# Performance work log

Hardware: AMD Instinct MI355X
Metric: run time of the kernel (lower is better)

Reference implementation:

```python
import jax, jax.numpy as jnp
import numpy as np

R = 10  # num_relations
NUM_GRAPHS = 64


def rgcn_layer(x, W, root, b, src, dst, etype):
    # x: [N, Din], W: [R, Din, H], root: [Din, H], b: [H]
    N = x.shape[0]
    H = W.shape[-1]
    # per-relation transform of all nodes: [R, N, H]
    h_all = jnp.einsum('nd,rdh->rnh', x, W)
    # gather transformed source features per edge by its relation: [E, H]
    msg = h_all[etype, src]
    # mean-aggregate per (dst, relation) pair, then sum over relations (PyG RGCNConv semantics)
    key = dst * R + etype
    sums = jax.ops.segment_sum(msg, key, num_segments=N * R)  # [N*R, H]
    cnt = jax.ops.segment_sum(jnp.ones((etype.shape[0],), x.dtype), key, num_segments=N * R)
    agg = (sums.reshape(N, R, H) / jnp.clip(cnt.reshape(N, R, 1), 1.0, None)).sum(axis=1)
    return agg + x @ root + b


def setup_inputs() -> dict:
    key = jax.random.key(0)
    ks = jax.random.split(key, 12)
    N, E, DIN, H = 100000, 3200000, 128, 64
    x = jax.random.normal(ks[0], (N, DIN), dtype=jnp.float32)
    edge_index = jax.random.randint(ks[1], (2, E), 0, N, dtype=jnp.int64)
    edge_type = jax.random.randint(ks[2], (E,), 0, R, dtype=jnp.int64)
    batch = jnp.sort(jax.random.randint(ks[3], (N,), 0, NUM_GRAPHS, dtype=jnp.int64))
    s1 = 1.0 / np.sqrt(DIN)
    s2 = 1.0 / np.sqrt(H)
    W1 = jax.random.uniform(ks[4], (R, DIN, H), jnp.float32, -s1, s1)
    root1 = jax.random.uniform(ks[5], (DIN, H), jnp.float32, -s1, s1)
    b1 = jnp.zeros((H,), jnp.float32)
    W2 = jax.random.uniform(ks[6], (R, H, H), jnp.float32, -s2, s2)
    root2 = jax.random.uniform(ks[7], (H, H), jnp.float32, -s2, s2)
    b2 = jnp.zeros((H,), jnp.float32)
    cls_w = jax.random.uniform(ks[8], (H, 1), jnp.float32, -s2, s2)
    cls_b = jnp.zeros((1,), jnp.float32)
    return {"x": x, "edge_index": edge_index, "edge_type": edge_type, "batch": batch,
            "W1": W1, "root1": root1, "b1": b1, "W2": W2, "root2": root2, "b2": b2,
            "cls_w": cls_w, "cls_b": cls_b}


def reference(x, edge_index, edge_type, batch, W1, root1, b1, W2, root2, b2, cls_w, cls_b):
    src, dst = edge_index[0], edge_index[1]
    h = jax.nn.relu(rgcn_layer(x, W1, root1, b1, src, dst, edge_type))   # dropout = identity (eval)
    h = jax.nn.relu(rgcn_layer(h, W2, root2, b2, src, dst, edge_type))
    # global mean pool per graph
    sums = jax.ops.segment_sum(h, batch, num_segments=NUM_GRAPHS)        # [G, H]
    cnt = jax.ops.segment_sum(jnp.ones((h.shape[0],), h.dtype), batch, num_segments=NUM_GRAPHS)
    pooled = sums / jnp.clip(cnt[:, None], 1.0, None)
    out = pooled @ cls_w + cls_b                                          # [G, 1]
    return out.reshape(-1)
```

## Files before the change

kernel.cpp:

```cpp
#include <hip/hip_runtime.h>

#define R_REL 10
#define HD 64
#define BSH 8
#define KPB (256 * R_REL)
#define SORT_CAP 12288

typedef __attribute__((ext_vector_type(8))) short short8;
typedef __attribute__((ext_vector_type(4))) float floatx4;
typedef __attribute__((ext_vector_type(8))) unsigned short ushort8;

__device__ inline unsigned short f32_to_bf16_rne(float f) {
    unsigned int u = __float_as_uint(f);
    unsigned int r = (u + 0x7FFFu + ((u >> 16) & 1u)) >> 16;
    return (unsigned short)r;
}
__device__ inline float bf16_to_f32(unsigned short h) {
    return __uint_as_float(((unsigned int)h) << 16);
}
__device__ inline float bf16lo(unsigned int u) { return __uint_as_float(u << 16); }
__device__ inline float bf16hi(unsigned int u) { return __uint_as_float(u & 0xFFFF0000u); }

__device__ __forceinline__ void gload_lds16(const unsigned short* g, unsigned short* l) {
    __builtin_amdgcn_global_load_lds(
        (const __attribute__((address_space(1))) unsigned int*)g,
        (__attribute__((address_space(3))) unsigned int*)l, 16, 0, 0);
}

#define BAR_VMCNT(N)                                              \
    do {                                                          \
        asm volatile("s_waitcnt vmcnt(" #N ")" ::: "memory");     \
        __builtin_amdgcn_sched_barrier(0);                        \
        __builtin_amdgcn_s_barrier();                             \
        __builtin_amdgcn_sched_barrier(0);                        \
    } while (0)

__global__ __launch_bounds__(256) void bhist_kernel(const int* __restrict__ dst,
                                                    int* __restrict__ bcnt, int E) {
    __shared__ int l[512];
    int t = threadIdx.x;
    l[t] = 0; l[t + 256] = 0;
    __syncthreads();
    int e0 = blockIdx.x * 4096;
    for (int i = t; i < 4096; i += 256) {
        int e = e0 + i;
        if (e < E) atomicAdd(&l[dst[e] >> BSH], 1);
    }
    __syncthreads();
    if (l[t]) atomicAdd(&bcnt[t], l[t]);
    if (l[t + 256]) atomicAdd(&bcnt[t + 256], l[t + 256]);
}

__global__ void bscan_kernel(const int* __restrict__ bcnt, int* __restrict__ boff,
                             int* __restrict__ gcursor, int NBK, int E) {
    int t = threadIdx.x;
    int v = (t < NBK) ? bcnt[t] : 0;
    __shared__ int tmp[512];
    tmp[t] = v;
    __syncthreads();
    for (int off = 1; off < 512; off <<= 1) {
        int u = (t >= off) ? tmp[t - off] : 0;
        __syncthreads();
        tmp[t] += u;
        __syncthreads();
    }
    int excl = tmp[t] - v;
    if (t < NBK) { boff[t] = excl; gcursor[t] = excl; }
    if (t == 0) boff[NBK] = E;
}

__global__ __launch_bounds__(256) void bscatter_kernel(const int* __restrict__ src,
                                                       const int* __restrict__ dst,
                                                       const int* __restrict__ et,
                                                       int* __restrict__ gcursor,
                                                       unsigned int* __restrict__ staged,
                                                       int E) {
    __shared__ int lcnt[512];
    __shared__ int lstart[512];
    __shared__ int lbase[512];
    __shared__ int tmp[256];
    __shared__ unsigned int lbuf[4096];
    __shared__ unsigned short lbkt[4096];
    int t = threadIdx.x;
    int e0 = blockIdx.x * 4096;
    int nthis = min(4096, E - e0);
    lcnt[t] = 0; lcnt[t + 256] = 0;
    __syncthreads();
    for (int i = t; i < nthis; i += 256) atomicAdd(&lcnt[dst[e0 + i] >> BSH], 1);
    __syncthreads();
    int c0 = lcnt[2 * t], c1 = lcnt[2 * t + 1];
    int ps = c0 + c1;
    tmp[t] = ps;
    __syncthreads();
    for (int off = 1; off < 256; off <<= 1) {
        int u = (t >= off) ? tmp[t - off] : 0;
        __syncthreads();
        tmp[t] += u;
        __syncthreads();
    }
    int ex = tmp[t] - ps;
    lstart[2 * t] = ex; lstart[2 * t + 1] = ex + c0;
    lbase[2 * t]     = (c0 > 0) ? atomicAdd(&gcursor[2 * t], c0) : 0;
    lbase[2 * t + 1] = (c1 > 0) ? atomicAdd(&gcursor[2 * t + 1], c1) : 0;
    __syncthreads();
    lcnt[t] = 0; lcnt[t + 256] = 0;
    __syncthreads();
    for (int i = t; i < nthis; i += 256) {
        int dd = dst[e0 + i];
        int bk = dd >> BSH;
        int lk = (dd & ((1 << BSH) - 1)) * R_REL + et[e0 + i];
        unsigned int p = ((unsigned int)lk << 17) | (unsigned int)src[e0 + i];
        int pos = lstart[bk] + atomicAdd(&lcnt[bk], 1);
        lbuf[pos] = p; lbkt[pos] = (unsigned short)bk;
    }
    __syncthreads();
    for (int i = t; i < nthis; i += 256) {
        int bk = lbkt[i];
        staged[lbase[bk] + i - lstart[bk]] = lbuf[i];
    }
}

__global__ __launch_bounds__(256) void sortfill_kernel(const unsigned int* __restrict__ staged,
                                                       const int* __restrict__ boff,
                                                       int* __restrict__ dcnt,
                                                       int2* __restrict__ edata,
                                                       int N, int Ntot) {
    __shared__ int hist[KPB];
    __shared__ float wkey[KPB];
    __shared__ int part[256];
    __shared__ int lsrc[SORT_CAP];
    __shared__ unsigned short lkey[SORT_CAP];
    int t = threadIdx.x, b = blockIdx.x;
    int s0 = boff[b], s1 = boff[b + 1];
#pragma unroll
    for (int j = 0; j < KPB / 256; ++j) hist[t + j * 256] = 0;
    __syncthreads();
    for (int i = s0 + t; i < s1; i += 256)
        atomicAdd(&hist[staged[i] >> 17], 1);
    __syncthreads();
    int base = t * (KPB / 256);
    int c[KPB / 256];
    int s = 0;
#pragma unroll
    for (int j = 0; j < KPB / 256; ++j) {
        c[j] = hist[base + j]; s += c[j];
        wkey[base + j] = 1.0f / fmaxf((float)c[j], 1.0f);
    }
    int dglob = b * 256 + t;
    if (dglob < Ntot) dcnt[dglob] = s;
    part[t] = s;
    __syncthreads();
    for (int off = 1; off < 256; off <<= 1) {
        int u = (t >= off) ? part[t - off] : 0;
        __syncthreads();
        part[t] += u;
        __syncthreads();
    }
    int run = part[t] - s;
#pragma unroll
    for (int j = 0; j < KPB / 256; ++j) { hist[base + j] = run; run += c[j]; }
    __syncthreads();
    for (int i = s0 + t; i < s1; i += 256) {
        unsigned int p = staged[i];
        int lk = p >> 17;
        int pos = atomicAdd(&hist[lk], 1);
        if (pos < SORT_CAP) { lsrc[pos] = (int)(p & 0x1FFFFu); lkey[pos] = (unsigned short)lk; }
        else {
            int rel = lk % R_REL;
            edata[s0 + pos] = make_int2(rel * N + (int)(p & 0x1FFFFu), __float_as_int(wkey[lk]));
        }
    }
    __syncthreads();
    int m = min(s1 - s0, SORT_CAP);
    for (int j = t; j < m; j += 256) {
        int lk = lkey[j];
        int rel = lk % R_REL;
        edata[s0 + j] = make_int2(rel * N + lsrc[j], __float_as_int(wkey[lk]));
    }
}

__global__ void scan1_kernel(const int* __restrict__ cnt, int* __restrict__ bsum, int M) {
    int b = blockIdx.x, tid = threadIdx.x;
    int base = b * 1024 + tid * 4;
    int s = 0;
#pragma unroll
    for (int j = 0; j < 4; ++j) { int i = base + j; if (i < M) s += cnt[i]; }
    for (int off = 32; off > 0; off >>= 1) s += __shfl_down(s, off);
    __shared__ int wsum[4];
    int lane = tid & 63, wid = tid >> 6;
    if (lane == 0) wsum[wid] = s;
    __syncthreads();
    if (tid == 0) bsum[b] = wsum[0] + wsum[1] + wsum[2] + wsum[3];
}

__global__ void scan2_kernel(const int* __restrict__ bsum, int* __restrict__ boff, int NB) {
    int tid = threadIdx.x;
    int lane = tid & 63, wid = tid >> 6;
    int v = (tid < NB) ? bsum[tid] : 0;
    int x = v;
    for (int off = 1; off < 64; off <<= 1) { int u = __shfl_up(x, off); if (lane >= off) x += u; }
    __shared__ int wsum[16];
    if (lane == 63) wsum[wid] = x;
    __syncthreads();
    int woff = 0;
    for (int w = 0; w < wid; ++w) woff += wsum[w];
    if (tid < NB) boff[tid] = x + woff - v;
}

__global__ void scan3_kernel(const int* __restrict__ cnt, const int* __restrict__ boff,
                             int* __restrict__ rowptr, int M) {
    int b = blockIdx.x, tid = threadIdx.x;
    int base = b * 1024 + tid * 4;
    int c[4]; int s = 0;
#pragma unroll
    for (int j = 0; j < 4; ++j) { int i = base + j; c[j] = (i < M) ? cnt[i] : 0; s += c[j]; }
    int lane = tid & 63, wid = tid >> 6;
    int x = s;
    for (int off = 1; off < 64; off <<= 1) { int u = __shfl_up(x, off); if (lane >= off) x += u; }
    __shared__ int wsum[4];
    if (lane == 63) wsum[wid] = x;
    __syncthreads();
    int woff = 0;
    for (int w = 0; w < wid; ++w) woff += wsum[w];
    int run = boff[b] + x + woff - s;
#pragma unroll
    for (int j = 0; j < 4; ++j) {
        int i = base + j;
        if (i < M) {
            rowptr[i] = run; run += c[j];
            if (i == M - 1) rowptr[M] = run;
        }
    }
}

__global__ void split_kernel(const float* __restrict__ src, unsigned short* __restrict__ hi,
                             unsigned short* __restrict__ lo, int n) {
    int i = blockIdx.x * 256 + threadIdx.x;
    if (i < n) {
        float v = src[i];
        unsigned short h = f32_to_bf16_rne(v);
        hi[i] = h;
        lo[i] = f32_to_bf16_rne(v - bf16_to_f32(h));
    }
}

__global__ void wsplit_kernel(const float* __restrict__ W, const float* __restrict__ root,
                              unsigned short* __restrict__ hi, int K) {
    int idx = blockIdx.x * 256 + threadIdx.x;
    int total = (R_REL + 1) * HD * K;
    if (idx >= total) return;
    int rel = idx / (HD * K);
    int rem = idx - rel * HD * K;
    int n = rem / K, k = rem - n * K;
    float v = (rel < R_REL) ? W[((size_t)rel * K + k) * HD + n] : root[(size_t)k * HD + n];
    int ks = k ^ ((n & 7) << 3);
    hi[rel * HD * K + n * K + ks] = f32_to_bf16_rne(v);
}

template <int K>
__global__ __launch_bounds__(512, 6)
void gemm_mfma(const unsigned short* __restrict__ Xhi,
               const unsigned short* __restrict__ Xlo,
               const unsigned short* __restrict__ Wthi,
               unsigned short* __restrict__ hout,
               float* __restrict__ fout, int N) {
    constexpr int NS = K / 32;
    constexpr int TILE_SH = HD * K;
    constexpr int SC = K / 64;
    __shared__ unsigned short wlds[2 * TILE_SH];
    const int tid = threadIdx.x;
    const int w = tid >> 6, lane = tid & 63;
    const int quad = lane >> 4, l16 = lane & 15;
    const int n0 = blockIdx.x * 128;
    const int node = n0 + w * 16 + l16;
    const bool valid = node < N;
    const bool full = (n0 + 128 <= N);

    short8 Xh[NS], Xl[NS];
#pragma unroll
    for (int s = 0; s < NS; ++s) {
        short8 z;
#pragma unroll
        for (int q = 0; q < 8; ++q) z[q] = 0;
        Xh[s] = z; Xl[s] = z;
        if (valid) {
            Xh[s] = *(const short8*)(Xhi + (size_t)node * K + s * 32 + quad * 8);
            Xl[s] = *(const short8*)(Xlo + (size_t)node * K + s * 32 + quad * 8);
        }
    }

    auto stage = [&](int rel, int b) {
        const unsigned short* hsrc = Wthi + (size_t)rel * TILE_SH;
        unsigned short* dst0 = wlds + b * TILE_SH;
#pragma unroll
        for (int j = 0; j < SC; ++j) {
            int q = j * 8 + w;
            gload_lds16(hsrc + q * 512 + lane * 8, dst0 + q * 512);
        }
    };

    stage(0, 0);
    BAR_VMCNT(0);

    const int swzb = (l16 & 7) << 4;
    const size_t NHD = (size_t)N * HD;

#pragma unroll
    for (int c = 0; c <= R_REL; ++c) {
        const int cur = c & 1;
        if (c < R_REL) stage(c + 1, cur ^ 1);
        const char* wb = (const char*)(wlds + cur * TILE_SH);
        floatx4 acc[4];
#pragma unroll
        for (int mt = 0; mt < 4; ++mt) { floatx4 z = {0.f, 0.f, 0.f, 0.f}; acc[mt] = z; }
#pragma unroll
        for (int s = 0; s < NS; ++s) {
            const int koffb = ((s * 32 + quad * 8) * 2) ^ swzb;
#pragma unroll
            for (int mt = 0; mt < 4; ++mt) {
                const int rowb = (mt * 16 + l16) * (K * 2);
                short8 Wh = *(const short8*)(wb + rowb + koffb);
                acc[mt] = __builtin_amdgcn_mfma_f32_16x16x32_bf16(Wh, Xh[s], acc[mt], 0, 0, 0);
                acc[mt] = __builtin_amdgcn_mfma_f32_16x16x32_bf16(Wh, Xl[s], acc[mt], 0, 0, 0);
            }
        }
        if (c < R_REL) {
            if (valid) {
                unsigned short* hp = hout + (size_t)c * NHD + (size_t)node * HD;
#pragma unroll
                for (int mt = 0; mt < 4; ++mt) {
                    unsigned int d0 = (unsigned int)f32_to_bf16_rne(acc[mt][0]) |
                                      ((unsigned int)f32_to_bf16_rne(acc[mt][1]) << 16);
                    unsigned int d1 = (unsigned int)f32_to_bf16_rne(acc[mt][2]) |
                                      ((unsigned int)f32_to_bf16_rne(acc[mt][3]) << 16);
                    *(uint2*)(hp + mt * 16 + quad * 4) = make_uint2(d0, d1);
                }
            }
        } else {
            if (valid) {
                float* fp = fout + (size_t)node * HD;
#pragma unroll
                for (int mt = 0; mt < 4; ++mt)
                    *(floatx4*)(fp + mt * 16 + quad * 4) = acc[mt];
            }
        }
        if (c < R_REL) {
            if (full) BAR_VMCNT(4); else BAR_VMCNT(0);
        }
    }
}

__global__ __launch_bounds__(256) void agg_kernel(const unsigned short* __restrict__ hc,
                                                  const int* __restrict__ rowptr,
                                                  const int2* __restrict__ edata,
                                                  float* __restrict__ acc, int N) {
    int gid = blockIdx.x * 256 + threadIdx.x;
    int d = gid >> 6;
    if (d >= N) return;
    int lane = threadIdx.x & 63;
    int quarter = lane >> 4, l16 = lane & 15;
    int e0 = rowptr[d], e1 = rowptr[d + 1];
    int ne = e1 - e0;
    if (ne == 0) return;
    float s0 = 0.f, s1 = 0.f, s2 = 0.f, s3 = 0.f;
    for (int rb = 0; rb < ne; rb += 64) {
        int nthis = min(64, ne - rb);
        int2 ed = make_int2(0, 0);
        if (lane < nthis) ed = edata[e0 + rb + lane];
        int off = ed.x << 6;
        float wv = __int_as_float(ed.y);
        for (int j = 0; j < nthis; j += 8) {
            int   oa = __shfl(off, j + quarter);
            float wa = __shfl(wv,  j + quarter);
            int   ob = __shfl(off, j + 4 + quarter);
            float wb = __shfl(wv,  j + 4 + quarter);
            uint2 da = *(const uint2*)(hc + oa + l16 * 4);
            uint2 db = *(const uint2*)(hc + ob + l16 * 4);
            s0 += wa * bf16lo(da.x); s1 += wa * bf16hi(da.x);
            s2 += wa * bf16lo(da.y); s3 += wa * bf16hi(da.y);
            s0 += wb * bf16lo(db.x); s1 += wb * bf16hi(db.x);
            s2 += wb * bf16lo(db.y); s3 += wb * bf16hi(db.y);
        }
    }
    s0 += __shfl_xor(s0, 16); s1 += __shfl_xor(s1, 16);
    s2 += __shfl_xor(s2, 16); s3 += __shfl_xor(s3, 16);
    s0 += __shfl_xor(s0, 32); s1 += __shfl_xor(s1, 32);
    s2 += __shfl_xor(s2, 32); s3 += __shfl_xor(s3, 32);
    if (lane < 16) {
        float4* ap = (float4*)(acc + (size_t)d * HD + l16 * 4);
        float4 a = *ap;
        a.x += s0; a.y += s1; a.z += s2; a.w += s3;
        *ap = a;
    }
}

__global__ void fin1_kernel(const float* __restrict__ acc, const float* __restrict__ bias,
                            unsigned short* __restrict__ hi, unsigned short* __restrict__ lo,
                            int NH) {
    int i = blockIdx.x * 256 + threadIdx.x;
    if (i < NH) {
        float v = fmaxf(acc[i] + bias[i & (HD - 1)], 0.f);
        unsigned short h = f32_to_bf16_rne(v);
        hi[i] = h;
        lo[i] = f32_to_bf16_rne(v - bf16_to_f32(h));
    }
}

__global__ __launch_bounds__(256) void pool_kernel(const float* __restrict__ acc,
                                                   const float* __restrict__ bias,
                                                   const int* __restrict__ batch,
                                                   float* __restrict__ pooled,
                                                   float* __restrict__ gcnt, int N) {
    int w = blockIdx.x * 4 + (threadIdx.x >> 6);
    int lane = threadIdx.x & 63;
    int base = w * 64;
    if (base >= N) return;
    int nn = min(64, N - base);
    float b = bias[lane];
    int g_l = (base + lane < N) ? batch[base + lane] : -1;
    int g_first = __shfl(g_l, 0);
    int g_last = __shfl(g_l, nn - 1);
    if (nn == 64 && g_first == g_last) {
        float p0 = 0.f, p1 = 0.f, p2 = 0.f, p3 = 0.f;
#pragma unroll
        for (int i = 0; i < 64; i += 4) {
            p0 += fmaxf(acc[(size_t)(base + i + 0) * HD + lane] + b, 0.f);
            p1 += fmaxf(acc[(size_t)(base + i + 1) * HD + lane] + b, 0.f);
            p2 += fmaxf(acc[(size_t)(base + i + 2) * HD + lane] + b, 0.f);
            p3 += fmaxf(acc[(size_t)(base + i + 3) * HD + lane] + b, 0.f);
        }
        atomicAdd(&pooled[g_first * HD + lane], (p0 + p1) + (p2 + p3));
        if (lane == 0) atomicAdd(&gcnt[g_first], 64.f);
    } else {
        int cur = g_first; float s = 0.f; int cnt = 0;
        for (int i = 0; i < nn; ++i) {
            int g = __shfl(g_l, i);
            if (g != cur) {
                atomicAdd(&pooled[cur * HD + lane], s);
                if (lane == 0) atomicAdd(&gcnt[cur], (float)cnt);
                cur = g; s = 0.f; cnt = 0;
            }
            s += fmaxf(acc[(size_t)(base + i) * HD + lane] + b, 0.f);
            cnt++;
        }
        atomicAdd(&pooled[cur * HD + lane], s);
        if (lane == 0) atomicAdd(&gcnt[cur], (float)cnt);
    }
}

__global__ void cls_kernel(const float* __restrict__ pooled, const float* __restrict__ gcnt,
                           const float* __restrict__ cls_w, const float* __restrict__ cls_b,
                           float* __restrict__ out) {
    int g = threadIdx.x;
    float invc = 1.0f / fmaxf(gcnt[g], 1.0f);
    float acc = 0.f;
    for (int j = 0; j < 64; ++j) acc += pooled[g * 64 + j] * cls_w[j];
    out[g] = acc * invc + cls_b[0];
}

extern "C" void kernel_launch(void* const* d_in, const int* in_sizes, int n_in,
                              void* d_out, int out_size, void* d_ws, size_t ws_size,
                              hipStream_t stream) {
    const float* x     = (const float*)d_in[0];
    const int*   eidx  = (const int*)d_in[1];
    const int*   et    = (const int*)d_in[2];
    const int*   batch = (const int*)d_in[3];
    const float* W1    = (const float*)d_in[4];
    const float* root1 = (const float*)d_in[5];
    const float* b1    = (const float*)d_in[6];
    const float* W2    = (const float*)d_in[7];
    const float* root2 = (const float*)d_in[8];
    const float* b2    = (const float*)d_in[9];
    const float* cls_w = (const float*)d_in[10];
    const float* cls_b = (const float*)d_in[11];

    const int N = in_sizes[3];
    const int E = in_sizes[2];
    const int NB = (N + 1023) / 1024;
    const int NBK = (N + (1 << BSH) - 1) >> BSH;
    const int* srcp = eidx;
    const int* dstp = eidx + E;

    char* ws = (char*)d_ws;
    size_t off = 0;
    auto alloc = [&](size_t bytes) -> void* {
        void* p = ws + off;
        off = (off + bytes + 255) & ~(size_t)255;
        return p;
    };
    unsigned short* Xhi  = (unsigned short*)alloc((size_t)N * 128 * 2);
    unsigned short* Xlo  = (unsigned short*)alloc((size_t)N * 128 * 2);
    float*          accb = (float*)alloc((size_t)N * HD * 4);
    unsigned short* Wt1hi = (unsigned short*)alloc((size_t)(R_REL + 1) * HD * 128 * 2);
    unsigned short* Wt2hi = (unsigned short*)alloc((size_t)(R_REL + 1) * HD * HD * 2);
    int2*  edata  = (int2*)alloc((size_t)E * 8);
    int*   rowptr = (int*)alloc((size_t)(N + 1) * 4);
    int*   dcnt   = (int*)alloc((size_t)N * 4);
    int*   bsum   = (int*)alloc((size_t)NB * 4);
    int*   bofs   = (int*)alloc((size_t)NB * 4);
    int*   bcnt   = (int*)alloc(512 * 4);
    int*   bboff  = (int*)alloc(513 * 4);
    int*   gcur   = (int*)alloc(512 * 4);
    float* pooled = (float*)alloc((size_t)(64 * HD + 64) * 4);
    float* gcnt   = pooled + 64 * HD;
    unsigned short* h_chunk = (unsigned short*)alloc((size_t)R_REL * N * HD * 2);

    unsigned int* staged = (unsigned int*)Xhi;
    unsigned short* H1hi = Xhi;
    unsigned short* H1lo = Xlo;

    hipMemsetAsync(bcnt, 0, 512 * 4, stream);
    hipMemsetAsync(pooled, 0, (size_t)(64 * HD + 64) * 4, stream);

    int nchunks = (E + 4095) / 4096;
    bhist_kernel<<<nchunks, 256, 0, stream>>>(dstp, bcnt, E);
    bscan_kernel<<<1, 512, 0, stream>>>(bcnt, bboff, gcur, NBK, E);
    bscatter_kernel<<<nchunks, 256, 0, stream>>>(srcp, dstp, et, gcur, staged, E);
    sortfill_kernel<<<NBK, 256, 0, stream>>>(staged, bboff, dcnt, edata, N, N);
    scan1_kernel<<<NB, 256, 0, stream>>>(dcnt, bsum, N);
    scan2_kernel<<<1, 1024, 0, stream>>>(bsum, bofs, NB);
    scan3_kernel<<<NB, 256, 0, stream>>>(dcnt, bofs, rowptr, N);

    int NK = N * 128;
    split_kernel<<<(NK + 255) / 256, 256, 0, stream>>>(x, Xhi, Xlo, NK);
    int tw1 = (R_REL + 1) * HD * 128, tw2 = (R_REL + 1) * HD * HD;
    wsplit_kernel<<<(tw1 + 255) / 256, 256, 0, stream>>>(W1, root1, Wt1hi, 128);
    wsplit_kernel<<<(tw2 + 255) / 256, 256, 0, stream>>>(W2, root2, Wt2hi, HD);

    const int gemmBlocks = (N + 127) / 128;
    const int aggBlocks  = (int)(((size_t)N * 64 + 255) / 256);
    const int NH = N * HD;

    gemm_mfma<128><<<gemmBlocks, 512, 0, stream>>>(Xhi, Xlo, Wt1hi, h_chunk, accb, N);
    agg_kernel<<<aggBlocks, 256, 0, stream>>>(h_chunk, rowptr, edata, accb, N);
    fin1_kernel<<<(NH + 255) / 256, 256, 0, stream>>>(accb, b1, H1hi, H1lo, NH);

    gemm_mfma<64><<<gemmBlocks, 512, 0, stream>>>(H1hi, H1lo, Wt2hi, h_chunk, accb, N);
    agg_kernel<<<aggBlocks, 256, 0, stream>>>(h_chunk, rowptr, edata, accb, N);

    int poolWaves = (N + 63) / 64;
    pool_kernel<<<(poolWaves + 3) / 4, 256, 0, stream>>>(accb, b2, batch, pooled, gcnt, N);
    cls_kernel<<<1, 64, 0, stream>>>(pooled, gcnt, cls_w, cls_b, (float*)d_out);
}
```

Baseline: 570.2 us.

## Compress edge records and fuse bias/ReLU/split and pooling into aggregation

Edge records shrink from 8-byte (offset, weight) pairs to a packed 4-byte (relation, src) word. The mean weights move into a per-(dst, relation) table that each wave loads once and shares across lanes by shuffle. The aggregation kernel now applies bias and ReLU directly. In layer 1 it writes the bf16 hi/lo split, and in layer 2 it atomically adds into the pooled sums, which removes the separate fin1 and pool kernels and a full pass over the accumulator. Graph counts come from a small new kernel. The trade-off is one atomic per node-feature into only 64 graph rows, which may contend heavily.

```diff
diff --git a/kernel.cpp b/kernel.cpp
--- a/kernel.cpp
+++ b/kernel.cpp
@@ -123,10 +123,10 @@
 __global__ __launch_bounds__(256) void sortfill_kernel(const unsigned int* __restrict__ staged,
                                                        const int* __restrict__ boff,
                                                        int* __restrict__ dcnt,
-                                                       int2* __restrict__ edata,
+                                                       unsigned int* __restrict__ edata,
+                                                       float* __restrict__ wrow,
                                                        int N, int Ntot) {
     __shared__ int hist[KPB];
-    __shared__ float wkey[KPB];
     __shared__ int part[256];
     __shared__ int lsrc[SORT_CAP];
     __shared__ unsigned short lkey[SORT_CAP];
@@ -144,7 +144,7 @@
 #pragma unroll
     for (int j = 0; j < KPB / 256; ++j) {
         c[j] = hist[base + j]; s += c[j];
-        wkey[base + j] = 1.0f / fmaxf((float)c[j], 1.0f);
+        wrow[b * KPB + base + j] = 1.0f / fmaxf((float)c[j], 1.0f);
     }
     int dglob = b * 256 + t;
     if (dglob < Ntot) dcnt[dglob] = s;
@@ -167,7 +167,7 @@
         if (pos < SORT_CAP) { lsrc[pos] = (int)(p & 0x1FFFFu); lkey[pos] = (unsigned short)lk; }
         else {
             int rel = lk % R_REL;
-            edata[s0 + pos] = make_int2(rel * N + (int)(p & 0x1FFFFu), __float_as_int(wkey[lk]));
+            edata[s0 + pos] = ((unsigned int)rel << 20) | (p & 0x1FFFFu);
         }
     }
     __syncthreads();
@@ -175,7 +175,7 @@
     for (int j = t; j < m; j += 256) {
         int lk = lkey[j];
         int rel = lk % R_REL;
-        edata[s0 + j] = make_int2(rel * N + lsrc[j], __float_as_int(wkey[lk]));
+        edata[s0 + j] = ((unsigned int)rel << 20) | (unsigned int)lsrc[j];
     }
 }
 
@@ -255,6 +255,21 @@
     float v = (rel < R_REL) ? W[((size_t)rel * K + k) * HD + n] : root[(size_t)k * HD + n];
     int ks = k ^ ((n & 7) << 3);
     hi[rel * HD * K + n * K + ks] = f32_to_bf16_rne(v);
+}
+
+__global__ __launch_bounds__(256) void gcnt_kernel(const int* __restrict__ batch,
+                                                   float* __restrict__ gcnt, int N) {
+    __shared__ int h[64];
+    int t = threadIdx.x;
+    if (t < 64) h[t] = 0;
+    __syncthreads();
+    int i0 = blockIdx.x * 4096;
+    for (int i = t; i < 4096; i += 256) {
+        int n = i0 + i;
+        if (n < N) atomicAdd(&h[batch[n]], 1);
+    }
+    __syncthreads();
+    if (t < 64 && h[t]) atomicAdd(&gcnt[t], (float)h[t]);
 }
 
 template <int K>
@@ -350,25 +365,35 @@
     }
 }
 
+template <int MODE>
 __global__ __launch_bounds__(256) void agg_kernel(const unsigned short* __restrict__ hc,
                                                   const int* __restrict__ rowptr,
-                                                  const int2* __restrict__ edata,
-                                                  float* __restrict__ acc, int N) {
+                                                  const unsigned int* __restrict__ edata,
+                                                  const float* __restrict__ wrow,
+                                                  const float* __restrict__ accb,
+                                                  const float* __restrict__ bias,
+                                                  const int* __restrict__ batch,
+                                                  unsigned short* __restrict__ hi,
+                                                  unsigned short* __restrict__ lo,
+                                                  float* __restrict__ pooled,
+                                                  int N) {
     int gid = blockIdx.x * 256 + threadIdx.x;
     int d = gid >> 6;
     if (d >= N) return;
     int lane = threadIdx.x & 63;
     int quarter = lane >> 4, l16 = lane & 15;
+    float w10 = (lane < R_REL) ? wrow[d * R_REL + lane] : 0.f;
     int e0 = rowptr[d], e1 = rowptr[d + 1];
     int ne = e1 - e0;
-    if (ne == 0) return;
     float s0 = 0.f, s1 = 0.f, s2 = 0.f, s3 = 0.f;
     for (int rb = 0; rb < ne; rb += 64) {
         int nthis = min(64, ne - rb);
-        int2 ed = make_int2(0, 0);
-        if (lane < nthis) ed = edata[e0 + rb + lane];
-        int off = ed.x << 6;
-        float wv = __int_as_float(ed.y);
+        unsigned int k = (lane < nthis) ? edata[e0 + rb + lane] : 0u;
+        int src = (int)(k & 0xFFFFFu);
+        int rel = (int)(k >> 20);
+        int off = (rel * N + src) << 6;
+        float wv = __shfl(w10, rel);
+        if (lane >= nthis) wv = 0.f;
         for (int j = 0; j < nthis; j += 8) {
             int   oa = __shfl(off, j + quarter);
             float wa = __shfl(wv,  j + quarter);
@@ -387,64 +412,30 @@
     s0 += __shfl_xor(s0, 32); s1 += __shfl_xor(s1, 32);
     s2 += __shfl_xor(s2, 32); s3 += __shfl_xor(s3, 32);
     if (lane < 16) {
-        float4* ap = (float4*)(acc + (size_t)d * HD + l16 * 4);
-        float4 a = *ap;
-        a.x += s0; a.y += s1; a.z += s2; a.w += s3;
-        *ap = a;
-    }
-}
-
-__global__ void fin1_kernel(const float* __restrict__ acc, const float* __restrict__ bias,
-                            unsigned short* __restrict__ hi, unsigned short* __restrict__ lo,
-                            int NH) {
-    int i = blockIdx.x * 256 + threadIdx.x;
-    if (i < NH) {
-        float v = fmaxf(acc[i] + bias[i & (HD - 1)], 0.f);
-        unsigned short h = f32_to_bf16_rne(v);
-        hi[i] = h;
-        lo[i] = f32_to_bf16_rne(v - bf16_to_f32(h));
-    }
-}
-
-__global__ __launch_bounds__(256) void pool_kernel(const float* __restrict__ acc,
-                                                   const float* __restrict__ bias,
-                                                   const int* __restrict__ batch,
-                                                   float* __restrict__ pooled,
-                                                   float* __restrict__ gcnt, int N) {
-    int w = blockIdx.x * 4 + (threadIdx.x >> 6);
-    int lane = threadIdx.x & 63;
-    int base = w * 64;
-    if (base >= N) return;
-    int nn = min(64, N - base);
-    float b = bias[lane];
-    int g_l = (base + lane < N) ? batch[base + lane] : -1;
-    int g_first = __shfl(g_l, 0);
-    int g_last = __shfl(g_l, nn - 1);
-    if (nn == 64 && g_first == g_last) {
-        float p0 = 0.f, p1 = 0.f, p2 = 0.f, p3 = 0.f;
-#pragma unroll
-        for (int i = 0; i < 64; i += 4) {
-            p0 += fmaxf(acc[(size_t)(base + i + 0) * HD + lane] + b, 0.f);
-            p1 += fmaxf(acc[(size_t)(base + i + 1) * HD + lane] + b, 0.f);
-            p2 += fmaxf(acc[(size_t)(base + i + 2) * HD + lane] + b, 0.f);
-            p3 += fmaxf(acc[(size_t)(base + i + 3) * HD + lane] + b, 0.f);
-        }
-        atomicAdd(&pooled[g_first * HD + lane], (p0 + p1) + (p2 + p3));
-        if (lane == 0) atomicAdd(&gcnt[g_first], 64.f);
-    } else {
-        int cur = g_first; float s = 0.f; int cnt = 0;
-        for (int i = 0; i < nn; ++i) {
-            int g = __shfl(g_l, i);
-            if (g != cur) {
-                atomicAdd(&pooled[cur * HD + lane], s);
-                if (lane == 0) atomicAdd(&gcnt[cur], (float)cnt);
-                cur = g; s = 0.f; cnt = 0;
-            }
-            s += fmaxf(acc[(size_t)(base + i) * HD + lane] + b, 0.f);
-            cnt++;
-        }
-        atomicAdd(&pooled[cur * HD + lane], s);
-        if (lane == 0) atomicAdd(&gcnt[cur], (float)cnt);
+        const float4 a = *(const float4*)(accb + (size_t)d * HD + l16 * 4);
+        const float4 b4 = *(const float4*)(bias + l16 * 4);
+        float v0 = fmaxf(a.x + s0 + b4.x, 0.f);
+        float v1 = fmaxf(a.y + s1 + b4.y, 0.f);
+        float v2 = fmaxf(a.z + s2 + b4.z, 0.f);
+        float v3 = fmaxf(a.w + s3 + b4.w, 0.f);
+        if (MODE == 0) {
+            unsigned short h0 = f32_to_bf16_rne(v0), h1 = f32_to_bf16_rne(v1);
+            unsigned short h2 = f32_to_bf16_rne(v2), h3 = f32_to_bf16_rne(v3);
+            unsigned short l0 = f32_to_bf16_rne(v0 - bf16_to_f32(h0));
+            unsigned short l1 = f32_to_bf16_rne(v1 - bf16_to_f32(h1));
+            unsigned short l2 = f32_to_bf16_rne(v2 - bf16_to_f32(h2));
+            unsigned short l3 = f32_to_bf16_rne(v3 - bf16_to_f32(h3));
+            size_t o = (size_t)d * HD + l16 * 4;
+            *(uint2*)(hi + o) = make_uint2((unsigned int)h0 | ((unsigned int)h1 << 16),
+                                           (unsigned int)h2 | ((unsigned int)h3 << 16));
+            *(uint2*)(lo + o) = make_uint2((unsigned int)l0 | ((unsigned int)l1 << 16),
+                                           (unsigned int)l2 | ((unsigned int)l3 << 16));
+        } else {
+            int g = batch[d];
+            float* pp = pooled + g * HD + l16 * 4;
+            atomicAdd(pp + 0, v0); atomicAdd(pp + 1, v1);
+            atomicAdd(pp + 2, v2); atomicAdd(pp + 3, v3);
+        }
     }
 }
 
@@ -493,7 +484,8 @@
     float*          accb = (float*)alloc((size_t)N * HD * 4);
     unsigned short* Wt1hi = (unsigned short*)alloc((size_t)(R_REL + 1) * HD * 128 * 2);
     unsigned short* Wt2hi = (unsigned short*)alloc((size_t)(R_REL + 1) * HD * HD * 2);
-    int2*  edata  = (int2*)alloc((size_t)E * 8);
+    unsigned int* edata  = (unsigned int*)alloc((size_t)E * 4);
+    float* wrow   = (float*)alloc((size_t)NBK * KPB * 4);
     int*   rowptr = (int*)alloc((size_t)(N + 1) * 4);
     int*   dcnt   = (int*)alloc((size_t)N * 4);
     int*   bsum   = (int*)alloc((size_t)NB * 4);
@@ -512,11 +504,13 @@
     hipMemsetAsync(bcnt, 0, 512 * 4, stream);
     hipMemsetAsync(pooled, 0, (size_t)(64 * HD + 64) * 4, stream);
 
+    gcnt_kernel<<<(N + 4095) / 4096, 256, 0, stream>>>(batch, gcnt, N);
+
     int nchunks = (E + 4095) / 4096;
     bhist_kernel<<<nchunks, 256, 0, stream>>>(dstp, bcnt, E);
     bscan_kernel<<<1, 512, 0, stream>>>(bcnt, bboff, gcur, NBK, E);
     bscatter_kernel<<<nchunks, 256, 0, stream>>>(srcp, dstp, et, gcur, staged, E);
-    sortfill_kernel<<<NBK, 256, 0, stream>>>(staged, bboff, dcnt, edata, N, N);
+    sortfill_kernel<<<NBK, 256, 0, stream>>>(staged, bboff, dcnt, edata, wrow, N, N);
     scan1_kernel<<<NB, 256, 0, stream>>>(dcnt, bsum, N);
     scan2_kernel<<<1, 1024, 0, stream>>>(bsum, bofs, NB);
     scan3_kernel<<<NB, 256, 0, stream>>>(dcnt, bofs, rowptr, N);
@@ -529,16 +523,15 @@
 
     const int gemmBlocks = (N + 127) / 128;
     const int aggBlocks  = (int)(((size_t)N * 64 + 255) / 256);
-    const int NH = N * HD;
 
     gemm_mfma<128><<<gemmBlocks, 512, 0, stream>>>(Xhi, Xlo, Wt1hi, h_chunk, accb, N);
-    agg_kernel<<<aggBlocks, 256, 0, stream>>>(h_chunk, rowptr, edata, accb, N);
-    fin1_kernel<<<(NH + 255) / 256, 256, 0, stream>>>(accb, b1, H1hi, H1lo, NH);
+    agg_kernel<0><<<aggBlocks, 256, 0, stream>>>(h_chunk, rowptr, edata, wrow, accb, b1,
+                                                 batch, H1hi, H1lo, pooled, N);
 
     gemm_mfma<64><<<gemmBlocks, 512, 0, stream>>>(H1hi, H1lo, Wt2hi, h_chunk, accb, N);
-    agg_kernel<<<aggBlocks, 256, 0, stream>>>(h_chunk, rowptr, edata, accb, N);
-
-    int poolWaves = (N + 63) / 64;
-    pool_kernel<<<(poolWaves + 3) / 4, 256, 0, stream>>>(accb, b2, batch, pooled, gcnt, N);
+    agg_kernel<1><<<aggBlocks, 256, 0, stream>>>(h_chunk, rowptr, edata, wrow, accb, b2,
+                                                 batch, (unsigned short*)nullptr,
+                                                 (unsigned short*)nullptr, pooled, N);
+
     cls_kernel<<<1, 64, 0, stream>>>(pooled, gcnt, cls_w, cls_b, (float*)d_out);
 }
```

Measured after the change: 1.157 ms. 103% more time.
